# Kernel tuning notes

Hardware: AMD Instinct MI355X
Metric: run time of the kernel (lower is better)

The kernel has to match this reference:

```python
import jax, jax.numpy as jnp
import numpy as np

B, C, H, W = 32, 3, 64, 64
KH, KW = 3, 3


def setup_inputs() -> dict:
    key = jax.random.key(0)
    x = jax.random.normal(key, (B, C, H, W), dtype=jnp.float32)
    return {"x": x}


def reference(x):
    b, c, h, w = x.shape
    hout, wout = h - KH + 1, w - KW + 1
    # im2col / nn.Unfold: torch orders the D=C*KH*KW axis channel-major:
    # index = c*KH*KW + i*KW + j
    patches = jnp.stack(
        [x[:, :, i:i + hout, j:j + wout] for i in range(KH) for j in range(KW)],
        axis=2,
    )  # [B, C, KH*KW, Hout, Wout]
    D = c * KH * KW
    p = patches.reshape(b, D, hout * wout).transpose(0, 2, 1)  # [B, L, D]
    # torch.combinations(row, 2, with_replacement=True) enumerates pairs
    # (i, j) with i <= j in lexicographic order == upper triangle row-major.
    ti, tj = jnp.triu_indices(D)
    feats = p[:, :, ti] * p[:, :, tj]  # [B, L, D*(D+1)//2]
    return feats.reshape(b, -1)
```

## Files before the change

kernel.cpp:

```cpp
#include <hip/hip_runtime.h>


#define B_    32
#define C_    3
#define H_    64
#define W_    64
#define HOUT  62
#define WOUT  62
#define L_    (HOUT * WOUT)
#define D_    27
#define NPAIR 378
#define NP2   189
#define NPOS  (B_ * L_)

__global__ __launch_bounds__(256) void localde_kernel(
    const float* __restrict__ x, float* __restrict__ out) {
  __shared__ unsigned int tab[NP2];
  __shared__ float pbuf[4][28];

  const int tid  = threadIdx.x;
  const int lane = tid & 63;
  const int wv   = tid >> 6;

  for (int t = tid; t < NP2; t += 256) {
    int pp = 2 * t;
    int i = 0, s = 0;
    while (s + (D_ - i) <= pp) { s += (D_ - i); ++i; }
    int j = i + (pp - s);
    unsigned int packed = (unsigned)i | ((unsigned)j << 8);
    ++pp;
    while (s + (D_ - i) <= pp) { s += (D_ - i); ++i; }
    j = i + (pp - s);
    packed |= ((unsigned)i << 16) | ((unsigned)j << 24);
    tab[t] = packed;
  }

  const int gidx = blockIdx.x * 4 + wv;
  if (gidx < NPOS && lane < D_) {
    int b  = gidx / L_;
    int l  = gidx - b * L_;
    int oh = l / WOUT;
    int ow = l - oh * WOUT;
    int c  = lane / 9;
    int r  = lane - c * 9;
    int ki = r / 3;
    int kj = r - ki * 3;
    pbuf[wv][lane] = x[((b * C_ + c) * H_ + oh + ki) * W_ + ow + kj];
  }
  __syncthreads();
  if (gidx >= NPOS) return;

  float2* __restrict__ outp = (float2*)(out + (size_t)gidx * NPAIR);
  const float* __restrict__ p = pbuf[wv];
#pragma unroll
  for (int t = 0; t < 3; ++t) {
    int pp2 = lane + t * 64;
    if (pp2 < NP2) {
      unsigned int tw = tab[pp2];
      float2 v;
      v.x = p[tw & 255u] * p[(tw >> 8) & 255u];
      v.y = p[(tw >> 16) & 255u] * p[tw >> 24];
      outp[pp2] = v;
    }
  }
}

extern "C" void kernel_launch(void* const* d_in, const int* in_sizes, int n_in,
                              void* d_out, int out_size, void* d_ws, size_t ws_size,
                              hipStream_t stream) {
  const float* x = (const float*)d_in[0];
  float* out = (float*)d_out;
  const int grid = NPOS / 4;
  localde_kernel<<<grid, 256, 0, stream>>>(x, out);
}
```

Before: 38.38 us.

## Process two positions per wave with 16-byte nontemporal stores

Each block now handles 8 output positions instead of 4, with each wave writing two consecutive positions' 756 floats as 189 float4 stores instead of float2 stores. The pair table is expanded to one entry per pair, and patch loads are spread across 216 threads. Nontemporal stores are meant to avoid cache pollution on this write-bound output. In exchange, each element does more index arithmetic and LDS lookups, and the grid is halved.

```diff
diff --git a/kernel.cpp b/kernel.cpp
--- a/kernel.cpp
+++ b/kernel.cpp
@@ -10,57 +10,62 @@
 #define L_    (HOUT * WOUT)
 #define D_    27
 #define NPAIR 378
-#define NP2   189
+#define NQ4   189
 #define NPOS  (B_ * L_)
+
+typedef float f32x4 __attribute__((ext_vector_type(4)));
 
 __global__ __launch_bounds__(256) void localde_kernel(
     const float* __restrict__ x, float* __restrict__ out) {
-  __shared__ unsigned int tab[NP2];
-  __shared__ float pbuf[4][28];
+  __shared__ unsigned int tab[NPAIR];
+  __shared__ float pbuf[8][28];
 
   const int tid  = threadIdx.x;
   const int lane = tid & 63;
   const int wv   = tid >> 6;
 
-  for (int t = tid; t < NP2; t += 256) {
-    int pp = 2 * t;
+  for (int t = tid; t < NPAIR; t += 256) {
     int i = 0, s = 0;
-    while (s + (D_ - i) <= pp) { s += (D_ - i); ++i; }
-    int j = i + (pp - s);
-    unsigned int packed = (unsigned)i | ((unsigned)j << 8);
-    ++pp;
-    while (s + (D_ - i) <= pp) { s += (D_ - i); ++i; }
-    j = i + (pp - s);
-    packed |= ((unsigned)i << 16) | ((unsigned)j << 24);
-    tab[t] = packed;
+    while (s + (D_ - i) <= t) { s += (D_ - i); ++i; }
+    int j = i + (t - s);
+    tab[t] = (unsigned)i | ((unsigned)j << 8);
   }
 
-  const int gidx = blockIdx.x * 4 + wv;
-  if (gidx < NPOS && lane < D_) {
+  if (tid < 8 * D_) {
+    int pos  = tid / D_;
+    int elem = tid - pos * D_;
+    int gidx = blockIdx.x * 8 + pos;
     int b  = gidx / L_;
     int l  = gidx - b * L_;
     int oh = l / WOUT;
     int ow = l - oh * WOUT;
-    int c  = lane / 9;
-    int r  = lane - c * 9;
+    int c  = elem / 9;
+    int r  = elem - c * 9;
     int ki = r / 3;
     int kj = r - ki * 3;
-    pbuf[wv][lane] = x[((b * C_ + c) * H_ + oh + ki) * W_ + ow + kj];
+    pbuf[pos][elem] = x[((b * C_ + c) * H_ + oh + ki) * W_ + ow + kj];
   }
   __syncthreads();
-  if (gidx >= NPOS) return;
 
-  float2* __restrict__ outp = (float2*)(out + (size_t)gidx * NPAIR);
-  const float* __restrict__ p = pbuf[wv];
+  const int g0 = blockIdx.x * 8 + wv * 2;
+  f32x4* __restrict__ outp = (f32x4*)(out + (size_t)g0 * NPAIR);
+  const float* __restrict__ pb = &pbuf[wv * 2][0];
+
 #pragma unroll
   for (int t = 0; t < 3; ++t) {
-    int pp2 = lane + t * 64;
-    if (pp2 < NP2) {
-      unsigned int tw = tab[pp2];
-      float2 v;
-      v.x = p[tw & 255u] * p[(tw >> 8) & 255u];
-      v.y = p[(tw >> 16) & 255u] * p[tw >> 24];
-      outp[pp2] = v;
+    int q = lane + t * 64;
+    if (q < NQ4) {
+      f32x4 v;
+#pragma unroll
+      for (int k = 0; k < 4; ++k) {
+        int e  = 4 * q + k;
+        int hi = (e >= NPAIR) ? 1 : 0;
+        int ee = e - hi * NPAIR;
+        unsigned tw = tab[ee];
+        const float* pp = pb + hi * 28;
+        v[k] = pp[tw & 255u] * pp[(tw >> 8) & 255u];
+      }
+      __builtin_nontemporal_store(v, &outp[q]);
     }
   }
 }
@@ -70,6 +75,6 @@
                               hipStream_t stream) {
   const float* x = (const float*)d_in[0];
   float* out = (float*)d_out;
-  const int grid = NPOS / 4;
+  const int grid = NPOS / 8;
   localde_kernel<<<grid, 256, 0, stream>>>(x, out);
 }
```

New measurement: 46.48 us. +21.1%, slower.

## Replace shared-memory pair table with wave readlane broadcast, two positions per wave

Applied to the files above, without the earlier changes.

Drops the shared pair-index table, the shared patch buffer and the block barrier. Each half-wave now holds one output position's 27 patch values in registers, and row i is broadcast with readlane, so each lane writes one element of the upper-triangle row per iteration. Packing two positions per wave halves the grid. The trade is scalar 4-byte stores with shrinking active lanes per row (27 iterations) in place of coalesced float2 stores, which may cut store efficiency.

```diff
diff --git a/kernel.cpp b/kernel.cpp
--- a/kernel.cpp
+++ b/kernel.cpp
@@ -10,58 +10,40 @@
 #define L_    (HOUT * WOUT)
 #define D_    27
 #define NPAIR 378
-#define NP2   189
 #define NPOS  (B_ * L_)
 
 __global__ __launch_bounds__(256) void localde_kernel(
     const float* __restrict__ x, float* __restrict__ out) {
-  __shared__ unsigned int tab[NP2];
-  __shared__ float pbuf[4][28];
-
   const int tid  = threadIdx.x;
   const int lane = tid & 63;
   const int wv   = tid >> 6;
+  const int half = lane >> 5;
+  const int j    = lane & 31;
+  const int jj   = (j < D_) ? j : (D_ - 1);
 
-  for (int t = tid; t < NP2; t += 256) {
-    int pp = 2 * t;
-    int i = 0, s = 0;
-    while (s + (D_ - i) <= pp) { s += (D_ - i); ++i; }
-    int j = i + (pp - s);
-    unsigned int packed = (unsigned)i | ((unsigned)j << 8);
-    ++pp;
-    while (s + (D_ - i) <= pp) { s += (D_ - i); ++i; }
-    j = i + (pp - s);
-    packed |= ((unsigned)i << 16) | ((unsigned)j << 24);
-    tab[t] = packed;
-  }
+  const int pos = (blockIdx.x * 4 + wv) * 2 + half;
+  int b  = pos / L_;
+  int l  = pos - b * L_;
+  int oh = l / WOUT;
+  int ow = l - oh * WOUT;
 
-  const int gidx = blockIdx.x * 4 + wv;
-  if (gidx < NPOS && lane < D_) {
-    int b  = gidx / L_;
-    int l  = gidx - b * L_;
-    int oh = l / WOUT;
-    int ow = l - oh * WOUT;
-    int c  = lane / 9;
-    int r  = lane - c * 9;
-    int ki = r / 3;
-    int kj = r - ki * 3;
-    pbuf[wv][lane] = x[((b * C_ + c) * H_ + oh + ki) * W_ + ow + kj];
-  }
-  __syncthreads();
-  if (gidx >= NPOS) return;
+  int c  = jj / 9;
+  int r  = jj - c * 9;
+  int ki = r / 3;
+  int kj = r - ki * 3;
 
-  float2* __restrict__ outp = (float2*)(out + (size_t)gidx * NPAIR);
-  const float* __restrict__ p = pbuf[wv];
+  const float pj  = x[((b * C_ + c) * H_ + oh + ki) * W_ + ow + kj];
+  const int   pjb = __float_as_int(pj);
+
+  float* const base = out + (size_t)pos * NPAIR + j;
+
 #pragma unroll
-  for (int t = 0; t < 3; ++t) {
-    int pp2 = lane + t * 64;
-    if (pp2 < NP2) {
-      unsigned int tw = tab[pp2];
-      float2 v;
-      v.x = p[tw & 255u] * p[(tw >> 8) & 255u];
-      v.y = p[(tw >> 16) & 255u] * p[tw >> 24];
-      outp[pp2] = v;
-    }
+  for (int i = 0; i < D_; ++i) {
+    const int s = i * D_ - (i * (i - 1)) / 2;
+    int lo = __builtin_amdgcn_readlane(pjb, i);
+    int hi = __builtin_amdgcn_readlane(pjb, 32 + i);
+    float pi = __int_as_float(half ? hi : lo);
+    if (j >= i && j < D_) base[s - i] = pi * pj;
   }
 }
 
@@ -70,6 +52,6 @@
                               hipStream_t stream) {
   const float* x = (const float*)d_in[0];
   float* out = (float*)d_out;
-  const int grid = NPOS / 4;
+  const int grid = NPOS / 8;
   localde_kernel<<<grid, 256, 0, stream>>>(x, out);
 }
```

Result: faster. 37.43 us (-2.5%).
